# Kernel optimization log

Measured on AMD Instinct MI355X. Metric: run time of the kernel, lower is better.

Reference implementation:

```python
import jax, jax.numpy as jnp
import numpy as np

K, M = 25, 8
EPS_BN = 1e-5


def knn(x, k):
    # x: (B, C, N) -> idx of k nearest points per point: (B, N, k)
    xt = jnp.swapaxes(x, 1, 2)                         # (B, N, C)
    inner = jnp.einsum('bnc,bcm->bnm', xt, x)          # (B, N, N)
    xx = jnp.sum(x * x, axis=1)                        # (B, N)
    neg_d2 = 2.0 * inner - xx[:, :, None] - xx[:, None, :]
    return jax.lax.top_k(neg_d2, k)[1]


def vec_avg(x, k, m):
    # x: (B, C, N). knn in full feature space (as in source); cross products use
    # the first 3 channels (torch.cross requires 3-d vectors).
    idx = knn(x, k)                                    # (B, N, k)
    pts = jnp.swapaxes(x[:, :3, :], 1, 2)              # (B, N, 3)
    neigh = jax.vmap(lambda p, i: p[i])(pts, idx)      # (B, N, k, 3)
    vecs = neigh - pts[:, :, None, :]                  # (B, N, k, 3)
    ii, jj = np.triu_indices(k, 1)                     # P = k(k-1)/2 pairs
    cr = jnp.cross(vecs[:, :, ii, :], vecs[:, :, jj, :])  # (B, N, P, 3)
    sq = jnp.sum(cr * cr, axis=-1)
    nrm = jnp.sqrt(jnp.maximum(sq, 1e-24))
    valid = nrm > 1e-6
    unit = jnp.where(valid[..., None], cr / nrm[..., None], 0.0)  # (B, N, P, 3)
    # sim_i = sum_j |n_i . n_j| over valid unit normals
    sim = jnp.sum(jnp.abs(jnp.einsum('bnpd,bnqd->bnpq', unit, unit)), axis=-1)
    sim = jnp.where(valid, sim, -jnp.inf)
    top_idx = jax.lax.top_k(sim, m)[1]                 # (B, N, m)
    top = jnp.take_along_axis(unit, top_idx[..., None], axis=2)  # (B, N, m, 3)
    avg = jnp.mean(top, axis=2)                        # (B, N, 3)
    return avg / (jnp.linalg.norm(avg, axis=-1, keepdims=True) + 1e-6)


def bn_cn(y, g, b):  # y: (B, C, N); training-mode batch stats per channel
    mu = jnp.mean(y, axis=(0, 2), keepdims=True)
    var = jnp.var(y, axis=(0, 2), keepdims=True)
    return g[None, :, None] * (y - mu) * jax.lax.rsqrt(var + EPS_BN) + b[None, :, None]


def bn_b(y, g, b):  # y: (B, C)
    mu = jnp.mean(y, axis=0)
    var = jnp.var(y, axis=0)
    return g * (y - mu) * jax.lax.rsqrt(var + EPS_BN) + b


def gelu(y):
    return jax.nn.gelu(y, approximate=False)


def _forward(x, w1, g1, b1, w2, g2, b2, w3, g3, b3, w4, g4, b4, wl1, g5, b5, wl2, bl2):
    n1 = jnp.swapaxes(vec_avg(x, K, M), 1, 2)          # (B, 3, N)
    x1 = gelu(bn_cn(jnp.einsum('bcn,oc->bon', jnp.concatenate([x, n1], 1), w1), g1, b1))
    n2 = jnp.swapaxes(vec_avg(x1, K, M), 1, 2)
    x2 = gelu(bn_cn(jnp.einsum('bcn,oc->bon', jnp.concatenate([x1, n2], 1), w2), g2, b2))
    n3 = jnp.swapaxes(vec_avg(x2, K, M), 1, 2)
    x3 = gelu(bn_cn(jnp.einsum('bcn,oc->bon', jnp.concatenate([x2, n3], 1), w3), g3, b3))
    x4 = gelu(bn_cn(jnp.einsum('bcn,oc->bon', jnp.concatenate([x1, x2, x3], 1), w4), g4, b4))
    e = jnp.max(x4, axis=-1)                           # adaptive_max_pool1d -> (B, emb)
    h = gelu(bn_b(e @ wl1.T, g5, b5))                  # dropout: eval-mode identity
    return h @ wl2.T + bl2


def setup_inputs():
    key = jax.random.key(0)
    ks = jax.random.split(key, 8)
    B, N, EMB, OUT = 2, 512, 1024, 40
    f32 = jnp.float32
    return {
        'x': jax.random.normal(ks[0], (B, 3, N), f32),
        'w1': jax.random.normal(ks[1], (64, 6), f32) * 0.1,
        'g1': jnp.ones((64,), f32), 'b1': jnp.zeros((64,), f32),
        'w2': jax.random.normal(ks[2], (64, 67), f32) * 0.1,
        'g2': jnp.ones((64,), f32), 'b2': jnp.zeros((64,), f32),
        'w3': jax.random.normal(ks[3], (128, 67), f32) * 0.1,
        'g3': jnp.ones((128,), f32), 'b3': jnp.zeros((128,), f32),
        'w4': jax.random.normal(ks[4], (EMB, 256), f32) * 0.05,
        'g4': jnp.ones((EMB,), f32), 'b4': jnp.zeros((EMB,), f32),
        'wl1': jax.random.normal(ks[5], (256, EMB), f32) * 0.03,
        'g5': jnp.ones((256,), f32), 'b5': jnp.zeros((256,), f32),
        'wl2': jax.random.normal(ks[6], (OUT, 256), f32) * 0.05,
        'bl2': jnp.zeros((OUT,), f32),
    }


def reference(x, w1, g1, b1, w2, g2, b2, w3, g3, b3, w4, g4, b4, wl1, g5, b5, wl2, bl2):
    return _forward(x, w1, g1, b1, w2, g2, b2, w3, g3, b3, w4, g4, b4, wl1, g5, b5, wl2, bl2)
```

## Files before the change

kernel.cpp:

```cpp
#include <hip/hip_runtime.h>
#include <math.h>

#define NPTS  512
#define KNN   25
#define NPAIR 300
#define MTOP  8
#define BB    2

__device__ __forceinline__ float gelu_f(float x) {
    return 0.5f * x * (1.0f + erff(x * 0.70710678118654752440f));
}
__device__ __forceinline__ float qnanf() { return __int_as_float(0x7fc00000); }

__global__ __launch_bounds__(256) void knn_wave_kernel(const float* __restrict__ x, int C,
                                                       int* __restrict__ knn_idx) {
    const int lane = threadIdx.x & 63;
    const int wave = threadIdx.x >> 6;
    const int n = blockIdx.x * 4 + wave;
    const int b = blockIdx.y;
    const float* xb = x + (size_t)b * C * NPTS;

    float inner[8] = {0.f,0.f,0.f,0.f,0.f,0.f,0.f,0.f};
    float xx[8]    = {0.f,0.f,0.f,0.f,0.f,0.f,0.f,0.f};
    float xx_n = 0.0f;
    for (int c = 0; c < C; ++c) {
        float xcn = xb[c * NPTS + n];
        xx_n = fmaf(xcn, xcn, xx_n);
        const float* row = xb + c * NPTS + lane;
#pragma unroll
        for (int j = 0; j < 8; ++j) {
            float v = row[64 * j];
            inner[j] = fmaf(xcn, v, inner[j]);
            xx[j]    = fmaf(v, v, xx[j]);
        }
    }
    float d[8];
#pragma unroll
    for (int j = 0; j < 8; ++j) d[j] = 2.0f * inner[j] - xx_n - xx[j];

    int myout = 0;
    for (int k = 0; k < KNN; ++k) {
        float bv = -INFINITY; int bi = 0x7fffffff;
#pragma unroll
        for (int j = 0; j < 8; ++j) {
            float v = d[j]; int m = lane + 64 * j;
            bool better = (v > bv) || (v == bv && m < bi);
            bv = better ? v : bv; bi = better ? m : bi;
        }
#pragma unroll
        for (int s = 32; s > 0; s >>= 1) {
            float ov = __shfl_xor(bv, s);
            int   oi = __shfl_xor(bi, s);
            bool better = (ov > bv) || (ov == bv && oi < bi);
            bv = better ? ov : bv; bi = better ? oi : bi;
        }
        if (lane == k) myout = bi;
#pragma unroll
        for (int j = 0; j < 8; ++j)
            if ((lane + 64 * j) == bi) d[j] = qnanf();
    }
    if (lane < KNN) knn_idx[((size_t)b * NPTS + n) * KNN + lane] = myout;
}

__global__ __launch_bounds__(256) void vecavg_kernel(const float* __restrict__ x, int C,
                                                     const int* __restrict__ knn_idx,
                                                     float* __restrict__ nout) {
    __shared__ float vx[KNN], vy[KNN], vz[KNN];
    __shared__ float ux[NPAIR], uy[NPAIR], uz[NPAIR];
    __shared__ int   validf[NPAIR];
    __shared__ float sim[NPAIR];
    __shared__ unsigned char pii[NPAIR], pjj[NPAIR];
    __shared__ unsigned char takenf[NPAIR];
    __shared__ float pw[4];
    __shared__ int   pi[4];
    __shared__ int   chosen[MTOP];

    const int n = blockIdx.x;
    const int b = blockIdx.y;
    const int t = threadIdx.x;
    const int lane = t & 63;
    const int wv = t >> 6;
    const float* xb = x + (size_t)b * C * NPTS;

    if (t == 0) {
        int c = 0;
        for (int i = 0; i < KNN; ++i)
            for (int j = i + 1; j < KNN; ++j) { pii[c] = (unsigned char)i; pjj[c] = (unsigned char)j; ++c; }
    }
    if (t < KNN) {
        const float cx = xb[0 * NPTS + n], cy = xb[1 * NPTS + n], cz = xb[2 * NPTS + n];
        int m = knn_idx[((size_t)b * NPTS + n) * KNN + t];
        vx[t] = xb[0 * NPTS + m] - cx;
        vy[t] = xb[1 * NPTS + m] - cy;
        vz[t] = xb[2 * NPTS + m] - cz;
    }
    __syncthreads();

    for (int p = t; p < NPAIR; p += 256) {
        int i = pii[p], j = pjj[p];
        float ax = vx[i], ay = vy[i], az = vz[i];
        float bx = vx[j], by = vy[j], bz = vz[j];
        float crx = ay * bz - az * by;
        float cry = az * bx - ax * bz;
        float crz = ax * by - ay * bx;
        float sq  = crx * crx + cry * cry + crz * crz;
        float nrm = sqrtf(fmaxf(sq, 1e-24f));
        int   v   = nrm > 1e-6f;
        validf[p] = v;
        ux[p] = v ? crx / nrm : 0.0f;
        uy[p] = v ? cry / nrm : 0.0f;
        uz[p] = v ? crz / nrm : 0.0f;
    }
    __syncthreads();

    for (int p = t; p < NPAIR; p += 256) {
        float a = ux[p], bb2 = uy[p], c2 = uz[p];
        float s = 0.0f;
        for (int q = 0; q < NPAIR; ++q) {
            s += fabsf(a * ux[q] + bb2 * uy[q] + c2 * uz[q]);
        }
        sim[p] = validf[p] ? s : -INFINITY;
    }
    __syncthreads();

    for (int p = t; p < NPAIR; p += 256) takenf[p] = 0;
    __syncthreads();

    for (int k = 0; k < MTOP; ++k) {
        float bv = -INFINITY; int bi = 0x7fffffff;
        for (int p = t; p < NPAIR; p += 256) {
            float v = sim[p];
            bool ok = (takenf[p] == 0) && ((v > bv) || (v == bv && p < bi));
            bv = ok ? v : bv; bi = ok ? p : bi;
        }
#pragma unroll
        for (int s = 32; s > 0; s >>= 1) {
            float ov = __shfl_xor(bv, s);
            int   oi = __shfl_xor(bi, s);
            bool better = (ov > bv) || (ov == bv && oi < bi);
            bv = better ? ov : bv; bi = better ? oi : bi;
        }
        if (lane == 0) { pw[wv] = bv; pi[wv] = bi; }
        __syncthreads();
        if (t == 0) {
            float wbv = pw[0]; int wbi = pi[0];
#pragma unroll
            for (int w = 1; w < 4; ++w) {
                float ov = pw[w]; int oi = pi[w];
                bool better = (ov > wbv) || (ov == wbv && oi < wbi);
                wbv = better ? ov : wbv; wbi = better ? oi : wbi;
            }
            chosen[k] = wbi;
            takenf[wbi] = 1;
        }
        __syncthreads();
    }

    if (t == 0) {
        float sx = 0.0f, sy = 0.0f, sz = 0.0f;
        for (int k = 0; k < MTOP; ++k) {
            int c = chosen[k];
            sx += ux[c]; sy += uy[c]; sz += uz[c];
        }
        sx *= 0.125f; sy *= 0.125f; sz *= 0.125f;
        float nn = sqrtf(sx * sx + sy * sy + sz * sz);
        float d  = nn + 1e-6f;
        nout[((size_t)b * 3 + 0) * NPTS + n] = sx / d;
        nout[((size_t)b * 3 + 1) * NPTS + n] = sy / d;
        nout[((size_t)b * 3 + 2) * NPTS + n] = sz / d;
    }
}

__global__ __launch_bounds__(256) void conv_kernel(const float* __restrict__ A, int Ca,
                                                   const float* __restrict__ Bs, int Cb,
                                                   const float* __restrict__ Cs, int Cc,
                                                   const float* __restrict__ W,
                                                   float* __restrict__ y, int O) {
    int gid = blockIdx.x * blockDim.x + threadIdx.x;
    int n    = gid % NPTS;
    int rest = gid / NPTS;
    int og   = rest % (O / 4);
    int b    = rest / (O / 4);
    if (b >= BB) return;
    int o0 = og * 4;
    int Ct = Ca + Cb + Cc;
    const float* w0 = W + (size_t)o0 * Ct;
    const float* w1 = w0 + Ct;
    const float* w2 = w1 + Ct;
    const float* w3 = w2 + Ct;
    float a0 = 0.f, a1 = 0.f, a2 = 0.f, a3 = 0.f;

    const float* pa = A + (size_t)b * Ca * NPTS + n;
    for (int c = 0; c < Ca; ++c) {
        float v = pa[(size_t)c * NPTS];
        a0 = fmaf(w0[c], v, a0); a1 = fmaf(w1[c], v, a1);
        a2 = fmaf(w2[c], v, a2); a3 = fmaf(w3[c], v, a3);
    }
    if (Cb > 0) {
        const float* pb = Bs + (size_t)b * Cb * NPTS + n;
        for (int c = 0; c < Cb; ++c) {
            float v = pb[(size_t)c * NPTS];
            a0 = fmaf(w0[Ca + c], v, a0); a1 = fmaf(w1[Ca + c], v, a1);
            a2 = fmaf(w2[Ca + c], v, a2); a3 = fmaf(w3[Ca + c], v, a3);
        }
    }
    if (Cc > 0) {
        const float* pc = Cs + (size_t)b * Cc * NPTS + n;
        int base = Ca + Cb;
        for (int c = 0; c < Cc; ++c) {
            float v = pc[(size_t)c * NPTS];
            a0 = fmaf(w0[base + c], v, a0); a1 = fmaf(w1[base + c], v, a1);
            a2 = fmaf(w2[base + c], v, a2); a3 = fmaf(w3[base + c], v, a3);
        }
    }
    size_t out = ((size_t)b * O + o0) * NPTS + n;
    y[out]            = a0;
    y[out + NPTS]     = a1;
    y[out + 2 * NPTS] = a2;
    y[out + 3 * NPTS] = a3;
}

#define GO 64
#define GN 64
#define GK 16
__global__ __launch_bounds__(256) void conv4_gemm(const float* __restrict__ x1,
                                                  const float* __restrict__ x2,
                                                  const float* __restrict__ x3,
                                                  const float* __restrict__ W,
                                                  float* __restrict__ y) {
    __shared__ float Xs[GK][GN];
    __shared__ float Ws[GO][GK + 4];
    const int t = threadIdx.x;
    const int o0 = blockIdx.x * GO;
    const int n0 = blockIdx.y * GN;
    const int b  = blockIdx.z;
    const int tn = (t & 15) * 4;
    const int to = (t >> 4) * 4;
    float acc[4][4] = {};

    for (int kk = 0; kk < 256; kk += GK) {
        {
            int r = t >> 4, cc = kk + r;
            const float* src = (cc < 64)  ? (x1 + ((size_t)b * 64  + cc)       * NPTS)
                             : (cc < 128) ? (x2 + ((size_t)b * 64  + (cc-64))  * NPTS)
                                          : (x3 + ((size_t)b * 128 + (cc-128)) * NPTS);
            *(float4*)&Xs[r][(t & 15) * 4] = *(const float4*)&src[n0 + (t & 15) * 4];
        }
        {
            int r = t >> 2;
            *(float4*)&Ws[r][(t & 3) * 4] =
                *(const float4*)&W[(size_t)(o0 + r) * 256 + kk + (t & 3) * 4];
        }
        __syncthreads();
#pragma unroll
        for (int k = 0; k < GK; ++k) {
            float4 xv = *(const float4*)&Xs[k][tn];
            float w0 = Ws[to + 0][k], w1 = Ws[to + 1][k];
            float w2 = Ws[to + 2][k], w3 = Ws[to + 3][k];
            acc[0][0] = fmaf(w0, xv.x, acc[0][0]); acc[0][1] = fmaf(w0, xv.y, acc[0][1]);
            acc[0][2] = fmaf(w0, xv.z, acc[0][2]); acc[0][3] = fmaf(w0, xv.w, acc[0][3]);
            acc[1][0] = fmaf(w1, xv.x, acc[1][0]); acc[1][1] = fmaf(w1, xv.y, acc[1][1]);
            acc[1][2] = fmaf(w1, xv.z, acc[1][2]); acc[1][3] = fmaf(w1, xv.w, acc[1][3]);
            acc[2][0] = fmaf(w2, xv.x, acc[2][0]); acc[2][1] = fmaf(w2, xv.y, acc[2][1]);
            acc[2][2] = fmaf(w2, xv.z, acc[2][2]); acc[2][3] = fmaf(w2, xv.w, acc[2][3]);
            acc[3][0] = fmaf(w3, xv.x, acc[3][0]); acc[3][1] = fmaf(w3, xv.y, acc[3][1]);
            acc[3][2] = fmaf(w3, xv.z, acc[3][2]); acc[3][3] = fmaf(w3, xv.w, acc[3][3]);
        }
        __syncthreads();
    }
#pragma unroll
    for (int i = 0; i < 4; ++i) {
        size_t base = ((size_t)b * 1024 + o0 + to + i) * NPTS + n0 + tn;
        float4 v = make_float4(acc[i][0], acc[i][1], acc[i][2], acc[i][3]);
        *(float4*)&y[base] = v;
    }
}

__global__ __launch_bounds__(256) void stats_kernel(const float* __restrict__ y, int O,
                                                    float* __restrict__ mean,
                                                    float* __restrict__ var) {
    const int o = blockIdx.x;
    const int t = threadIdx.x;
    __shared__ float ss[256], sq[256];
    float s = 0.f, q = 0.f;
    for (int i = t; i < BB * NPTS; i += 256) {
        int b = i / NPTS, n = i % NPTS;
        float v = y[((size_t)b * O + o) * NPTS + n];
        s += v; q += v * v;
    }
    ss[t] = s; sq[t] = q;
    __syncthreads();
    for (int st = 128; st > 0; st >>= 1) {
        if (t < st) { ss[t] += ss[t + st]; sq[t] += sq[t + st]; }
        __syncthreads();
    }
    if (t == 0) {
        float mu = ss[0] / (float)(BB * NPTS);
        mean[o] = mu;
        var[o]  = fmaxf(sq[0] / (float)(BB * NPTS) - mu * mu, 0.0f);
    }
}

__global__ __launch_bounds__(256) void bn_gelu_kernel(const float* __restrict__ y, int O,
                                                      const float* __restrict__ g,
                                                      const float* __restrict__ bb,
                                                      const float* __restrict__ mean,
                                                      const float* __restrict__ var,
                                                      float* __restrict__ out) {
    int gid = blockIdx.x * blockDim.x + threadIdx.x;
    int o = (gid / NPTS) % O;
    int b = gid / (NPTS * O);
    if (b >= BB) return;
    float v = y[gid];
    float z = g[o] * (v - mean[o]) * (1.0f / sqrtf(var[o] + 1e-5f)) + bb[o];
    out[gid] = gelu_f(z);
}

__global__ __launch_bounds__(256) void stats_bn_max_kernel(const float* __restrict__ y,
                                                           const float* __restrict__ g4,
                                                           const float* __restrict__ b4,
                                                           float* __restrict__ e) {
    const int o = blockIdx.x;
    const int t = threadIdx.x;
    __shared__ float ss[256], sq[256];
    __shared__ float stat[2];

    float v00 = y[((size_t)0 * 1024 + o) * NPTS + t];
    float v01 = y[((size_t)0 * 1024 + o) * NPTS + t + 256];
    float v10 = y[((size_t)1 * 1024 + o) * NPTS + t];
    float v11 = y[((size_t)1 * 1024 + o) * NPTS + t + 256];

    float s = v00 + v01 + v10 + v11;
    float q = v00 * v00 + v01 * v01 + v10 * v10 + v11 * v11;
    ss[t] = s; sq[t] = q;
    __syncthreads();
    for (int st = 128; st > 0; st >>= 1) {
        if (t < st) { ss[t] += ss[t + st]; sq[t] += sq[t + st]; }
        __syncthreads();
    }
    if (t == 0) {
        float mu = ss[0] / 1024.0f;
        stat[0] = mu;
        stat[1] = 1.0f / sqrtf(fmaxf(sq[0] / 1024.0f - mu * mu, 0.0f) + 1e-5f);
    }
    __syncthreads();
    float mu = stat[0], inv = stat[1];
    float gg = g4[o], bbv = b4[o];
    float m0 = fmaxf(gelu_f(gg * (v00 - mu) * inv + bbv),
                     gelu_f(gg * (v01 - mu) * inv + bbv));
    float m1 = fmaxf(gelu_f(gg * (v10 - mu) * inv + bbv),
                     gelu_f(gg * (v11 - mu) * inv + bbv));
    ss[t] = m0; sq[t] = m1;
    __syncthreads();
    for (int st = 128; st > 0; st >>= 1) {
        if (t < st) { ss[t] = fmaxf(ss[t], ss[t + st]); sq[t] = fmaxf(sq[t], sq[t + st]); }
        __syncthreads();
    }
    if (t == 0) { e[o] = ss[0]; e[1024 + o] = sq[0]; }
}

__global__ __launch_bounds__(256) void lin1_kernel(const float* __restrict__ e,
                                                   const float* __restrict__ wl1,
                                                   float* __restrict__ tb) {
    const int j = blockIdx.x;
    const int t = threadIdx.x;
    __shared__ float r0[256], r1[256];
    float4 w  = *(const float4*)&wl1[(size_t)j * 1024 + t * 4];
    float4 e0 = *(const float4*)&e[t * 4];
    float4 e1 = *(const float4*)&e[1024 + t * 4];
    float s0 = fmaf(w.w, e0.w, fmaf(w.z, e0.z, fmaf(w.y, e0.y, w.x * e0.x)));
    float s1 = fmaf(w.w, e1.w, fmaf(w.z, e1.z, fmaf(w.y, e1.y, w.x * e1.x)));
    r0[t] = s0; r1[t] = s1;
    __syncthreads();
    for (int s = 128; s > 0; s >>= 1) {
        if (t < s) { r0[t] += r0[t + s]; r1[t] += r1[t + s]; }
        __syncthreads();
    }
    if (t == 0) { tb[j] = r0[0]; tb[256 + j] = r1[0]; }
}

__global__ __launch_bounds__(256) void headh_kernel(const float* __restrict__ tb,
                                                    const float* __restrict__ g5,
                                                    const float* __restrict__ b5,
                                                    float* __restrict__ h) {
    int j = threadIdx.x;
    float t0 = tb[j], t1 = tb[256 + j];
    float mu = 0.5f * (t0 + t1);
    float d0 = t0 - mu, d1 = t1 - mu;
    float var = 0.5f * (d0 * d0 + d1 * d1);
    float inv = 1.0f / sqrtf(var + 1e-5f);
    h[j]       = gelu_f(g5[j] * d0 * inv + b5[j]);
    h[256 + j] = gelu_f(g5[j] * d1 * inv + b5[j]);
}

__global__ __launch_bounds__(128) void out_kernel(const float* __restrict__ h,
                                                  const float* __restrict__ wl2,
                                                  const float* __restrict__ bl2,
                                                  float* __restrict__ out) {
    int gid = blockIdx.x * blockDim.x + threadIdx.x;
    if (gid >= BB * 40) return;
    int o = gid % 40;
    int b = gid / 40;
    const float* hb = h + (size_t)b * 256;
    const float* w  = wl2 + (size_t)o * 256;
    float acc = 0.f;
    for (int j = 0; j < 256; ++j) acc = fmaf(hb[j], w[j], acc);
    out[gid] = acc + bl2[o];
}

extern "C" void kernel_launch(void* const* d_in, const int* in_sizes, int n_in,
                              void* d_out, int out_size, void* d_ws, size_t ws_size,
                              hipStream_t stream) {
    const float* x   = (const float*)d_in[0];
    const float* w1  = (const float*)d_in[1];
    const float* g1  = (const float*)d_in[2];
    const float* b1  = (const float*)d_in[3];
    const float* w2  = (const float*)d_in[4];
    const float* g2  = (const float*)d_in[5];
    const float* b2  = (const float*)d_in[6];
    const float* w3  = (const float*)d_in[7];
    const float* g3  = (const float*)d_in[8];
    const float* b3  = (const float*)d_in[9];
    const float* w4  = (const float*)d_in[10];
    const float* g4  = (const float*)d_in[11];
    const float* b4  = (const float*)d_in[12];
    const float* wl1 = (const float*)d_in[13];
    const float* g5  = (const float*)d_in[14];
    const float* b5  = (const float*)d_in[15];
    const float* wl2 = (const float*)d_in[16];
    const float* bl2 = (const float*)d_in[17];
    float* outp = (float*)d_out;

    char* base = (char*)d_ws;
    size_t off = 0;
    auto alloc = [&](size_t bytes) -> void* {
        void* p = base + off;
        off += (bytes + 255) & ~(size_t)255;
        return p;
    };
    int*   idxb  = (int*)  alloc((size_t)BB * NPTS * KNN * sizeof(int));
    float* nbuf  = (float*)alloc((size_t)BB * 3 * NPTS * sizeof(float));
    float* x1    = (float*)alloc((size_t)BB * 64 * NPTS * sizeof(float));
    float* x2    = (float*)alloc((size_t)BB * 64 * NPTS * sizeof(float));
    float* x3    = (float*)alloc((size_t)BB * 128 * NPTS * sizeof(float));
    float* ybuf  = (float*)alloc((size_t)BB * 1024 * NPTS * sizeof(float));
    float* meanb = (float*)alloc(1024 * sizeof(float));
    float* varb  = (float*)alloc(1024 * sizeof(float));
    float* eb    = (float*)alloc((size_t)BB * 1024 * sizeof(float));
    float* tb    = (float*)alloc((size_t)BB * 256 * sizeof(float));
    float* hb    = (float*)alloc((size_t)BB * 256 * sizeof(float));
    (void)ws_size; (void)in_sizes; (void)n_in; (void)out_size;

    dim3 va_grid(NPTS, BB);
    dim3 knn_wgrid(NPTS / 4, BB);

    auto layer = [&](const float* A, int Ca, const float* Bs, int Cb,
                     const float* Cs, int Cc, const float* W,
                     const float* g, const float* bb, int O, float* outbuf) {
        int total = BB * (O / 4) * NPTS;
        conv_kernel<<<total / 256, 256, 0, stream>>>(A, Ca, Bs, Cb, Cs, Cc, W, ybuf, O);
        stats_kernel<<<O, 256, 0, stream>>>(ybuf, O, meanb, varb);
        bn_gelu_kernel<<<(BB * O * NPTS) / 256, 256, 0, stream>>>(ybuf, O, g, bb, meanb, varb, outbuf);
    };

    knn_wave_kernel<<<knn_wgrid, 256, 0, stream>>>(x, 3, idxb);
    vecavg_kernel<<<va_grid, 256, 0, stream>>>(x, 3, idxb, nbuf);
    layer(x, 3, nbuf, 3, nullptr, 0, w1, g1, b1, 64, x1);
    knn_wave_kernel<<<knn_wgrid, 256, 0, stream>>>(x1, 64, idxb);
    vecavg_kernel<<<va_grid, 256, 0, stream>>>(x1, 64, idxb, nbuf);
    layer(x1, 64, nbuf, 3, nullptr, 0, w2, g2, b2, 64, x2);
    knn_wave_kernel<<<knn_wgrid, 256, 0, stream>>>(x2, 64, idxb);
    vecavg_kernel<<<va_grid, 256, 0, stream>>>(x2, 64, idxb, nbuf);
    layer(x2, 64, nbuf, 3, nullptr, 0, w3, g3, b3, 128, x3);
    conv4_gemm<<<dim3(1024 / GO, NPTS / GN, BB), 256, 0, stream>>>(x1, x2, x3, w4, ybuf);
    stats_bn_max_kernel<<<1024, 256, 0, stream>>>(ybuf, g4, b4, eb);

    lin1_kernel<<<256, 256, 0, stream>>>(eb, wl1, tb);
    headh_kernel<<<1, 256, 0, stream>>>(tb, g5, b5, hb);
    out_kernel<<<1, 128, 0, stream>>>(hb, wl2, bl2, outp);
    (void)meanb; (void)varb;
}
```

Baseline: 263.8 us.

## Fuse head BN-GELU with output linear and use one output per thread in conv

Merges the head batch-norm/GELU kernel and the final linear kernel into one launch, keeping the hidden activations in shared memory and dropping the hb workspace buffer. The point-wise conv kernel now computes one output channel per thread instead of four, which gives four times as many threads for more parallelism. The cost is that each input value is reloaded once per output channel rather than shared across four accumulators.

```diff
diff --git a/kernel.cpp b/kernel.cpp
--- a/kernel.cpp
+++ b/kernel.cpp
@@ -171,53 +171,33 @@
     }
 }
 
-__global__ __launch_bounds__(256) void conv_kernel(const float* __restrict__ A, int Ca,
-                                                   const float* __restrict__ Bs, int Cb,
-                                                   const float* __restrict__ Cs, int Cc,
-                                                   const float* __restrict__ W,
-                                                   float* __restrict__ y, int O) {
+__global__ __launch_bounds__(256) void conv_kernel1(const float* __restrict__ A, int Ca,
+                                                    const float* __restrict__ Bs, int Cb,
+                                                    const float* __restrict__ Cs, int Cc,
+                                                    const float* __restrict__ W,
+                                                    float* __restrict__ y, int O) {
     int gid = blockIdx.x * blockDim.x + threadIdx.x;
     int n    = gid % NPTS;
     int rest = gid / NPTS;
-    int og   = rest % (O / 4);
-    int b    = rest / (O / 4);
+    int o    = rest % O;
+    int b    = rest / O;
     if (b >= BB) return;
-    int o0 = og * 4;
     int Ct = Ca + Cb + Cc;
-    const float* w0 = W + (size_t)o0 * Ct;
-    const float* w1 = w0 + Ct;
-    const float* w2 = w1 + Ct;
-    const float* w3 = w2 + Ct;
-    float a0 = 0.f, a1 = 0.f, a2 = 0.f, a3 = 0.f;
+    const float* w = W + (size_t)o * Ct;
+    float a0 = 0.f;
 
     const float* pa = A + (size_t)b * Ca * NPTS + n;
-    for (int c = 0; c < Ca; ++c) {
-        float v = pa[(size_t)c * NPTS];
-        a0 = fmaf(w0[c], v, a0); a1 = fmaf(w1[c], v, a1);
-        a2 = fmaf(w2[c], v, a2); a3 = fmaf(w3[c], v, a3);
-    }
+    for (int c = 0; c < Ca; ++c) a0 = fmaf(w[c], pa[(size_t)c * NPTS], a0);
     if (Cb > 0) {
         const float* pb = Bs + (size_t)b * Cb * NPTS + n;
-        for (int c = 0; c < Cb; ++c) {
-            float v = pb[(size_t)c * NPTS];
-            a0 = fmaf(w0[Ca + c], v, a0); a1 = fmaf(w1[Ca + c], v, a1);
-            a2 = fmaf(w2[Ca + c], v, a2); a3 = fmaf(w3[Ca + c], v, a3);
-        }
+        for (int c = 0; c < Cb; ++c) a0 = fmaf(w[Ca + c], pb[(size_t)c * NPTS], a0);
     }
     if (Cc > 0) {
         const float* pc = Cs + (size_t)b * Cc * NPTS + n;
         int base = Ca + Cb;
-        for (int c = 0; c < Cc; ++c) {
-            float v = pc[(size_t)c * NPTS];
-            a0 = fmaf(w0[base + c], v, a0); a1 = fmaf(w1[base + c], v, a1);
-            a2 = fmaf(w2[base + c], v, a2); a3 = fmaf(w3[base + c], v, a3);
-        }
-    }
-    size_t out = ((size_t)b * O + o0) * NPTS + n;
-    y[out]            = a0;
-    y[out + NPTS]     = a1;
-    y[out + 2 * NPTS] = a2;
-    y[out + 3 * NPTS] = a3;
+        for (int c = 0; c < Cc; ++c) a0 = fmaf(w[base + c], pc[(size_t)c * NPTS], a0);
+    }
+    y[gid] = a0;
 }
 
 #define GO 64
@@ -379,33 +359,32 @@
     if (t == 0) { tb[j] = r0[0]; tb[256 + j] = r1[0]; }
 }
 
-__global__ __launch_bounds__(256) void headh_kernel(const float* __restrict__ tb,
-                                                    const float* __restrict__ g5,
-                                                    const float* __restrict__ b5,
-                                                    float* __restrict__ h) {
-    int j = threadIdx.x;
-    float t0 = tb[j], t1 = tb[256 + j];
-    float mu = 0.5f * (t0 + t1);
-    float d0 = t0 - mu, d1 = t1 - mu;
-    float var = 0.5f * (d0 * d0 + d1 * d1);
-    float inv = 1.0f / sqrtf(var + 1e-5f);
-    h[j]       = gelu_f(g5[j] * d0 * inv + b5[j]);
-    h[256 + j] = gelu_f(g5[j] * d1 * inv + b5[j]);
-}
-
-__global__ __launch_bounds__(128) void out_kernel(const float* __restrict__ h,
-                                                  const float* __restrict__ wl2,
-                                                  const float* __restrict__ bl2,
-                                                  float* __restrict__ out) {
-    int gid = blockIdx.x * blockDim.x + threadIdx.x;
-    if (gid >= BB * 40) return;
-    int o = gid % 40;
-    int b = gid / 40;
-    const float* hb = h + (size_t)b * 256;
-    const float* w  = wl2 + (size_t)o * 256;
-    float acc = 0.f;
-    for (int j = 0; j < 256; ++j) acc = fmaf(hb[j], w[j], acc);
-    out[gid] = acc + bl2[o];
+__global__ __launch_bounds__(256) void head_kernel(const float* __restrict__ tb,
+                                                   const float* __restrict__ g5,
+                                                   const float* __restrict__ b5,
+                                                   const float* __restrict__ wl2,
+                                                   const float* __restrict__ bl2,
+                                                   float* __restrict__ out) {
+    __shared__ float h0[256], h1[256];
+    const int j = threadIdx.x;
+    {
+        float t0 = tb[j], t1 = tb[256 + j];
+        float mu = 0.5f * (t0 + t1);
+        float d0 = t0 - mu, d1 = t1 - mu;
+        float var = 0.5f * (d0 * d0 + d1 * d1);
+        float inv = 1.0f / sqrtf(var + 1e-5f);
+        h0[j] = gelu_f(g5[j] * d0 * inv + b5[j]);
+        h1[j] = gelu_f(g5[j] * d1 * inv + b5[j]);
+    }
+    __syncthreads();
+    if (j < BB * 40) {
+        int o = j % 40, b = j / 40;
+        const float* hh = b ? h1 : h0;
+        const float* w  = wl2 + (size_t)o * 256;
+        float acc = 0.f;
+        for (int c = 0; c < 256; ++c) acc = fmaf(hh[c], w[c], acc);
+        out[j] = acc + bl2[o];
+    }
 }
 
 extern "C" void kernel_launch(void* const* d_in, const int* in_sizes, int n_in,
@@ -448,7 +427,6 @@
     float* varb  = (float*)alloc(1024 * sizeof(float));
     float* eb    = (float*)alloc((size_t)BB * 1024 * sizeof(float));
     float* tb    = (float*)alloc((size_t)BB * 256 * sizeof(float));
-    float* hb    = (float*)alloc((size_t)BB * 256 * sizeof(float));
     (void)ws_size; (void)in_sizes; (void)n_in; (void)out_size;
 
     dim3 va_grid(NPTS, BB);
@@ -457,8 +435,8 @@
     auto layer = [&](const float* A, int Ca, const float* Bs, int Cb,
                      const float* Cs, int Cc, const float* W,
                      const float* g, const float* bb, int O, float* outbuf) {
-        int total = BB * (O / 4) * NPTS;
-        conv_kernel<<<total / 256, 256, 0, stream>>>(A, Ca, Bs, Cb, Cs, Cc, W, ybuf, O);
+        int total = BB * O * NPTS;
+        conv_kernel1<<<total / 256, 256, 0, stream>>>(A, Ca, Bs, Cb, Cs, Cc, W, ybuf, O);
         stats_kernel<<<O, 256, 0, stream>>>(ybuf, O, meanb, varb);
         bn_gelu_kernel<<<(BB * O * NPTS) / 256, 256, 0, stream>>>(ybuf, O, g, bb, meanb, varb, outbuf);
     };
@@ -476,7 +454,5 @@
     stats_bn_max_kernel<<<1024, 256, 0, stream>>>(ybuf, g4, b4, eb);
 
     lin1_kernel<<<256, 256, 0, stream>>>(eb, wl1, tb);
-    headh_kernel<<<1, 256, 0, stream>>>(tb, g5, b5, hb);
-    out_kernel<<<1, 128, 0, stream>>>(hb, wl2, bl2, outp);
-    (void)meanb; (void)varb;
-}
+    head_kernel<<<1, 256, 0, stream>>>(tb, g5, b5, wl2, bl2, outp);
+}
```

Measured after the change: 260.4 us. About the same (-1.3%).
